# Kernel optimization log

Measured on AMD Instinct MI355X. Metric: run time of the kernel, lower is better.

## Reference

```python
import jax, jax.numpy as jnp
import numpy as np

B, T, D = 32, 4096, 256
P, K, L = 2, 17, 3
NH, HD, FF, HID = 8, 32, 2048, 128


def _ln(x, w, b):
    m = x.mean(-1, keepdims=True)
    v = ((x - m) ** 2).mean(-1, keepdims=True)
    return (x - m) * jax.lax.rsqrt(v + 1e-5) * w + b


def _refine(x, w1, b1, w2, b2):
    # x: (B,P,K,D). Vectorized all-pairs: pair[b,p,i,j] = concat(x_i, x_j); MLP; mean over j; residual.
    xi = jnp.broadcast_to(x[:, :, :, None, :], (B, P, K, K, D))
    xj = jnp.broadcast_to(x[:, :, None, :, :], (B, P, K, K, D))
    pair = jnp.concatenate([xi, xj], axis=-1)  # (B,P,K,K,2D)
    h = jax.nn.relu(pair @ w1.T + b1)
    y = (h @ w2.T + b2).mean(axis=3)  # (B,P,K,D)
    return y + x


def _forward(memory, person_q, key_q, sa_in_w, sa_in_b, sa_out_w, sa_out_b,
             ca_in_w, ca_in_b, ca_out_w, ca_out_b, ff1_w, ff1_b, ff2_w, ff2_b,
             ln1_w, ln1_b, ln2_w, ln2_b, ln3_w, ln3_b,
             r1_w1, r1_b1, r1_w2, r1_b2, r2_w1, r2_b1, r2_w2, r2_b2, fc_w, fc_b):
    scale = 1.0 / np.sqrt(HD).astype(np.float32)
    # tgt for person p = person_q[p] + key_q, all persons vectorized into axis P
    x = jnp.broadcast_to(person_q[None, :, None, :] + key_q[None, None, :, :], (B, P, K, D))
    for l in range(L):
        # --- self-attention over K keypoint queries (post-norm TransformerDecoderLayer) ---
        qkv = x @ sa_in_w[l].T + sa_in_b[l]
        q, k, v = jnp.split(qkv, 3, axis=-1)
        qh = q.reshape(B, P, K, NH, HD)
        kh = k.reshape(B, P, K, NH, HD)
        vh = v.reshape(B, P, K, NH, HD)
        a = jax.nn.softmax(jnp.einsum('bpqhd,bpkhd->bphqk', qh, kh) * scale, axis=-1)
        o = jnp.einsum('bphqk,bpkhd->bpqhd', a, vh).reshape(B, P, K, D)
        x = _ln(x + o @ sa_out_w[l].T + sa_out_b[l], ln1_w[l], ln1_b[l])
        # --- cross-attention to memory; memory K/V computed once, shared across persons ---
        q = x @ ca_in_w[l][:D].T + ca_in_b[l][:D]
        mk = memory @ ca_in_w[l][D:2 * D].T + ca_in_b[l][D:2 * D]
        mv = memory @ ca_in_w[l][2 * D:].T + ca_in_b[l][2 * D:]
        qh = q.reshape(B, P, K, NH, HD)
        kh = mk.reshape(B, T, NH, HD)
        vh = mv.reshape(B, T, NH, HD)
        a = jax.nn.softmax(jnp.einsum('bpqhd,bthd->bphqt', qh, kh) * scale, axis=-1)
        o = jnp.einsum('bphqt,bthd->bpqhd', a, vh).reshape(B, P, K, D)
        x = _ln(x + o @ ca_out_w[l].T + ca_out_b[l], ln2_w[l], ln2_b[l])
        # --- feed-forward (ReLU, dim_feedforward=2048 default) ---
        h = jax.nn.relu(x @ ff1_w[l].T + ff1_b[l])
        x = _ln(x + h @ ff2_w[l].T + ff2_b[l], ln3_w[l], ln3_b[l])
    x = _refine(x, r1_w1, r1_b1, r1_w2, r1_b2)
    x = _refine(x, r2_w1, r2_b1, r2_w2, r2_b2)
    return x @ fc_w.T + fc_b  # (B, P, K, 3)


def setup_inputs() -> dict:
    key = jax.random.key(0)
    ks = iter(jax.random.split(key, 48))

    def w(shape, s=0.02):
        return jax.random.normal(next(ks), shape, dtype=jnp.float32) * s

    inp = {
        'memory': jax.random.normal(next(ks), (B, T, D), dtype=jnp.float32),
        'person_q': jax.random.normal(next(ks), (P, D), dtype=jnp.float32),
        'key_q': jax.random.normal(next(ks), (K, D), dtype=jnp.float32),
        'sa_in_w': w((L, 3 * D, D)), 'sa_in_b': jnp.zeros((L, 3 * D)),
        'sa_out_w': w((L, D, D)), 'sa_out_b': jnp.zeros((L, D)),
        'ca_in_w': w((L, 3 * D, D)), 'ca_in_b': jnp.zeros((L, 3 * D)),
        'ca_out_w': w((L, D, D)), 'ca_out_b': jnp.zeros((L, D)),
        'ff1_w': w((L, FF, D)), 'ff1_b': jnp.zeros((L, FF)),
        'ff2_w': w((L, D, FF)), 'ff2_b': jnp.zeros((L, D)),
        'ln1_w': jnp.ones((L, D)), 'ln1_b': jnp.zeros((L, D)),
        'ln2_w': jnp.ones((L, D)), 'ln2_b': jnp.zeros((L, D)),
        'ln3_w': jnp.ones((L, D)), 'ln3_b': jnp.zeros((L, D)),
        'r1_w1': w((HID, 2 * D)), 'r1_b1': jnp.zeros((HID,)),
        'r1_w2': w((D, HID)), 'r1_b2': jnp.zeros((D,)),
        'r2_w1': w((HID, 2 * D)), 'r2_b1': jnp.zeros((HID,)),
        'r2_w2': w((D, HID)), 'r2_b2': jnp.zeros((D,)),
        'fc_w': w((3, D)), 'fc_b': jnp.zeros((3,)),
    }
    return inp


def reference(memory, person_q, key_q, sa_in_w, sa_in_b, sa_out_w, sa_out_b,
              ca_in_w, ca_in_b, ca_out_w, ca_out_b, ff1_w, ff1_b, ff2_w, ff2_b,
              ln1_w, ln1_b, ln2_w, ln2_b, ln3_w, ln3_b,
              r1_w1, r1_b1, r1_w2, r1_b2, r2_w1, r2_b1, r2_w2, r2_b2, fc_w, fc_b):
    return _forward(memory, person_q, key_q, sa_in_w, sa_in_b, sa_out_w, sa_out_b,
                    ca_in_w, ca_in_b, ca_out_w, ca_out_b, ff1_w, ff1_b, ff2_w, ff2_b,
                    ln1_w, ln1_b, ln2_w, ln2_b, ln3_w, ln3_b,
                    r1_w1, r1_b1, r1_w2, r1_b2, r2_w1, r2_b1, r2_w2, r2_b2, fc_w, fc_b)
```

## Files before the change

kernel.cpp:

```cpp
#include <hip/hip_runtime.h>
#include <stdint.h>

#define NB   32
#define TSEQ 4096
#define DD   256
#define PP   2
#define KK   17
#define LL   3
#define NHH  8
#define HDD  32
#define FFD  2048
#define HIDD 128
#define ROWS 1088
#define SCALE 0.17677669529663689f

typedef __attribute__((ext_vector_type(4))) float f32x4;
typedef __attribute__((ext_vector_type(8))) short bf16x8;

static __device__ __forceinline__ unsigned cvtpk(float lo, float hi) {
  unsigned r;
  asm volatile("v_cvt_pk_bf16_f32 %0, %1, %2" : "=v"(r) : "v"(lo), "v"(hi));
  return r;
}
static __device__ __forceinline__ unsigned short f2bf(float f) {
  unsigned int x = __float_as_uint(f);
  return (unsigned short)((x + 0x7fffu + ((x >> 16) & 1u)) >> 16);
}
static __device__ __forceinline__ void gload_lds16(const void* g, void* l) {
  __builtin_amdgcn_global_load_lds(
      (const __attribute__((address_space(1))) unsigned int*)g,
      (__attribute__((address_space(3))) unsigned int*)l, 16, 0, 0);
}

struct CvtJob { const float* src; unsigned short* dst; int n; };
struct CvtJobs8 { CvtJob j[8]; };
__global__ __launch_bounds__(256) void cvt_multi_kernel(CvtJobs8 jobs) {
#pragma unroll
  for (int jj = 0; jj < 8; ++jj) {
    const float* src = jobs.j[jj].src;
    unsigned short* dst = jobs.j[jj].dst;
    const int n8 = jobs.j[jj].n >> 3;
    for (int i = blockIdx.x * 256 + threadIdx.x; i < n8; i += gridDim.x * 256) {
      const float4 f0 = *reinterpret_cast<const float4*>(src + i * 8);
      const float4 f1 = *reinterpret_cast<const float4*>(src + i * 8 + 4);
      uint4 st;
      st.x = cvtpk(f0.x, f0.y); st.y = cvtpk(f0.z, f0.w);
      st.z = cvtpk(f1.x, f1.y); st.w = cvtpk(f1.z, f1.w);
      *reinterpret_cast<uint4*>(dst + i * 8) = st;
    }
  }
}

__global__ __launch_bounds__(256) void prep_small_kernel(
    const float* __restrict__ person_q, const float* __restrict__ key_q,
    const float* __restrict__ ca_in_w, const float* __restrict__ ca_in_b,
    const float* __restrict__ ca_out_w, const float* __restrict__ ca_out_b,
    float* __restrict__ x, unsigned short* __restrict__ x_bf,
    float* __restrict__ bqk, float* __restrict__ bvo) {
  const int bx = blockIdx.x, tid = threadIdx.x;
  if (bx < ROWS) {
    const int p = (bx / KK) & 1, k = bx % KK;
    const float v = person_q[p * DD + tid] + key_q[k * DD + tid];
    x[(size_t)bx * DD + tid] = v;
    x_bf[(size_t)bx * DD + tid] = f2bf(v);
  } else if (bx < ROWS + 24) {
    const int b2 = bx - ROWS;
    const int l = b2 >> 3, h = b2 & 7;
    const float* Wk = ca_in_w + (size_t)l * 196608 + (size_t)(256 + h * 32) * 256;
    const float* bq = ca_in_b + l * 768 + h * 32;
    float acc = 0.f;
#pragma unroll
    for (int j = 0; j < 32; ++j) acc += bq[j] * Wk[(size_t)j * 256 + tid];
    bqk[(size_t)l * 2048 + h * 256 + tid] = acc * SCALE;
  } else {
    const int l = bx - ROWS - 24;
    float acc = ca_out_b[l * 256 + tid];
    for (int j = 0; j < 256; ++j)
      acc += ca_out_w[(size_t)l * 65536 + (size_t)tid * 256 + j] * ca_in_b[l * 768 + 512 + j];
    bvo[l * 256 + tid] = acc;
  }
}

__global__ __launch_bounds__(256) void gemm_bf16_kernel(
    const unsigned short* __restrict__ Xbf, const unsigned short* __restrict__ Wbf,
    const float* __restrict__ bias, const float* __restrict__ R,
    float* __restrict__ Yf, unsigned short* __restrict__ Ybf,
    int M, int N, int K, int wstride, int relu) {
  __shared__ unsigned short Xs[64 * 64];
  __shared__ unsigned short Ws[64 * 64];
  const int tid = threadIdx.x, lane = tid & 63, w = tid >> 6;
  const int g = lane >> 4, q16 = lane & 15;
  const int m0 = blockIdx.y * 64, n0 = blockIdx.x * 64;
  f32x4 acc[4];
#pragma unroll
  for (int nt = 0; nt < 4; ++nt) acc[nt] = (f32x4){0.f, 0.f, 0.f, 0.f};

  for (int k0 = 0; k0 < K; k0 += 64) {
    __syncthreads();
#pragma unroll
    for (int j = 0; j < 2; ++j) {
      const int cc = w * 2 + j;
      const int row = cc * 8 + (lane >> 3);
      const int sc = (lane & 7) ^ (row & 7);
      gload_lds16(Xbf + (size_t)(m0 + row) * K + k0 + sc * 8, &Xs[cc * 512]);
      gload_lds16(Wbf + (size_t)(n0 + row) * wstride + k0 + sc * 8, &Ws[cc * 512]);
    }
    asm volatile("s_waitcnt vmcnt(0)" ::: "memory");
    __syncthreads();
    const int arow = w * 16 + q16;
#pragma unroll
    for (int ks = 0; ks < 2; ++ks) {
      const bf16x8 a = *reinterpret_cast<const bf16x8*>(
          &Xs[arow * 64 + ((((ks << 2) + g) ^ (arow & 7)) << 3)]);
#pragma unroll
      for (int nt = 0; nt < 4; ++nt) {
        const int brow = nt * 16 + q16;
        const bf16x8 bfr = *reinterpret_cast<const bf16x8*>(
            &Ws[brow * 64 + ((((ks << 2) + g) ^ (brow & 7)) << 3)]);
        acc[nt] = __builtin_amdgcn_mfma_f32_16x16x32_bf16(a, bfr, acc[nt], 0, 0, 0);
      }
    }
  }
#pragma unroll
  for (int nt = 0; nt < 4; ++nt) {
    const int n = n0 + nt * 16 + q16;
    const float bv = bias ? bias[n] : 0.f;
#pragma unroll
    for (int r = 0; r < 4; ++r) {
      const int m = m0 + w * 16 + g * 4 + r;
      float o = acc[nt][r] + bv;
      if (relu) o = fmaxf(o, 0.f);
      if (R) o += R[(size_t)m * N + n];
      if (Yf) Yf[(size_t)m * N + n] = o;
      if (Ybf) Ybf[(size_t)m * N + n] = f2bf(o);
    }
  }
}

__global__ __launch_bounds__(256) void gemm_bf16_sk_kernel(
    const unsigned short* __restrict__ Xbf, const unsigned short* __restrict__ Wbf,
    float* __restrict__ part, int M, int N, int K, int wstride, int kslice) {
  __shared__ unsigned short Xs[64 * 64];
  __shared__ unsigned short Ws[64 * 64];
  const int tid = threadIdx.x, lane = tid & 63, w = tid >> 6;
  const int g = lane >> 4, q16 = lane & 15;
  const int m0 = blockIdx.y * 64, n0 = blockIdx.x * 64;
  const int kz = blockIdx.z;
  const int kbeg = kz * kslice, kend = kbeg + kslice;
  f32x4 acc[4];
#pragma unroll
  for (int nt = 0; nt < 4; ++nt) acc[nt] = (f32x4){0.f, 0.f, 0.f, 0.f};

  for (int k0 = kbeg; k0 < kend; k0 += 64) {
    __syncthreads();
#pragma unroll
    for (int j = 0; j < 2; ++j) {
      const int cc = w * 2 + j;
      const int row = cc * 8 + (lane >> 3);
      const int sc = (lane & 7) ^ (row & 7);
      gload_lds16(Xbf + (size_t)(m0 + row) * K + k0 + sc * 8, &Xs[cc * 512]);
      gload_lds16(Wbf + (size_t)(n0 + row) * wstride + k0 + sc * 8, &Ws[cc * 512]);
    }
    asm volatile("s_waitcnt vmcnt(0)" ::: "memory");
    __syncthreads();
    const int arow = w * 16 + q16;
#pragma unroll
    for (int ks = 0; ks < 2; ++ks) {
      const bf16x8 a = *reinterpret_cast<const bf16x8*>(
          &Xs[arow * 64 + ((((ks << 2) + g) ^ (arow & 7)) << 3)]);
#pragma unroll
      for (int nt = 0; nt < 4; ++nt) {
        const int brow = nt * 16 + q16;
        const bf16x8 bfr = *reinterpret_cast<const bf16x8*>(
            &Ws[brow * 64 + ((((ks << 2) + g) ^ (brow & 7)) << 3)]);
        acc[nt] = __builtin_amdgcn_mfma_f32_16x16x32_bf16(a, bfr, acc[nt], 0, 0, 0);
      }
    }
  }
  float* pout = part + (size_t)kz * M * N;
#pragma unroll
  for (int nt = 0; nt < 4; ++nt) {
    const int n = n0 + nt * 16 + q16;
#pragma unroll
    for (int r = 0; r < 4; ++r) {
      const int m = m0 + w * 16 + g * 4 + r;
      pout[(size_t)m * N + n] = acc[nt][r];
    }
  }
}

__global__ __launch_bounds__(256) void ln_red_kernel(
    const float* __restrict__ xin, const float* __restrict__ parts, int np,
    const float* __restrict__ bias, const float* __restrict__ w,
    const float* __restrict__ b, float* __restrict__ xout,
    unsigned short* __restrict__ xout_bf) {
  const int row = blockIdx.x, tid = threadIdx.x;
  const size_t base = (size_t)row * DD + tid;
  float v = xin[base] + bias[tid];
  for (int p = 0; p < np; ++p) v += parts[(size_t)p * ROWS * DD + base];
  float s = v, s2 = v * v;
#pragma unroll
  for (int off = 32; off > 0; off >>= 1) {
    s += __shfl_down(s, off);
    s2 += __shfl_down(s2, off);
  }
  __shared__ float ps[4], ps2[4];
  if ((tid & 63) == 0) { ps[tid >> 6] = s; ps2[tid >> 6] = s2; }
  __syncthreads();
  const float st = ps[0] + ps[1] + ps[2] + ps[3];
  const float st2 = ps2[0] + ps2[1] + ps2[2] + ps2[3];
  const float mean = st * (1.f / 256.f);
  const float var = st2 * (1.f / 256.f) - mean * mean;
  const float inv = rsqrtf(var + 1e-5f);
  const float o = (v - mean) * inv * w[tid] + b[tid];
  xout[base] = o;
  xout_bf[base] = f2bf(o);
}

__global__ __launch_bounds__(256) void fc_kernel(
    const float* __restrict__ x, const float* __restrict__ fc_w,
    const float* __restrict__ fc_b, float* __restrict__ out) {
  const int row = blockIdx.x * 4 + (threadIdx.x >> 6);
  const int lane = threadIdx.x & 63;
  float xr[4];
#pragma unroll
  for (int j = 0; j < 4; ++j) xr[j] = x[(size_t)row * DD + lane + 64 * j];
#pragma unroll
  for (int o = 0; o < 3; ++o) {
    float s = 0.f;
#pragma unroll
    for (int j = 0; j < 4; ++j) s += xr[j] * fc_w[o * DD + lane + 64 * j];
#pragma unroll
    for (int off = 32; off > 0; off >>= 1) s += __shfl_down(s, off);
    if (lane == 0) out[(size_t)row * 3 + o] = s + fc_b[o];
  }
}

__global__ __launch_bounds__(64) void sa_attn_kernel(
    const float* __restrict__ qkv, unsigned short* __restrict__ attn_bf) {
  const int blk = blockIdx.x;
  const int h = blk & 7, bp = blk >> 3;
  const int rowbase = bp * KK;
  const int tid = threadIdx.x;
  __shared__ float qs[KK][36], ks[KK][36], vs[KK][36];
  __shared__ float ss[KK][20];
  __shared__ float lsum[KK];
  for (int i = tid; i < KK * HDD; i += 64) {
    const int r = i >> 5, d = i & 31;
    const size_t base = (size_t)(rowbase + r) * 768 + h * 32 + d;
    qs[r][d] = qkv[base];
    ks[r][d] = qkv[base + 256];
    vs[r][d] = qkv[base + 512];
  }
  __syncthreads();
  for (int i = tid; i < KK * KK; i += 64) {
    const int q = i / KK, k = i % KK;
    float s = 0.f;
#pragma unroll
    for (int d = 0; d < HDD; ++d) s += qs[q][d] * ks[k][d];
    ss[q][k] = s * SCALE;
  }
  __syncthreads();
  if (tid < KK) {
    float m = -1e30f;
    for (int k = 0; k < KK; ++k) m = fmaxf(m, ss[tid][k]);
    float l = 0.f;
    for (int k = 0; k < KK; ++k) { const float e = __expf(ss[tid][k] - m); ss[tid][k] = e; l += e; }
    lsum[tid] = l;
  }
  __syncthreads();
  for (int i = tid; i < KK * HDD; i += 64) {
    const int q = i >> 5, d = i & 31;
    float o = 0.f;
#pragma unroll
    for (int k = 0; k < KK; ++k) o += ss[q][k] * vs[k][d];
    attn_bf[(size_t)(rowbase + q) * DD + h * 32 + d] = f2bf(o / lsum[q]);
  }
}

__global__ __launch_bounds__(256) void wqkvo_kernel(
    const float* __restrict__ ca_in_w, const float* __restrict__ ca_out_w,
    unsigned short* __restrict__ Wqk_bf, unsigned short* __restrict__ Wvo_bf) {
  const int bx0 = blockIdx.x;
  if (bx0 < 6144) {
    const int l = bx0 >> 11, hc = bx0 & 2047;
    const int h = hc >> 8, c = hc & 255;
    const int d = threadIdx.x;
    const float* Wq = ca_in_w + (size_t)l * 196608 + (size_t)(h * 32) * 256;
    const float* Wk = ca_in_w + (size_t)l * 196608 + (size_t)(256 + h * 32) * 256;
    float acc = 0.f;
#pragma unroll
    for (int j = 0; j < 32; ++j) acc += Wk[(size_t)j * 256 + c] * Wq[(size_t)j * 256 + d];
    Wqk_bf[((size_t)l * 2048 + hc) * 256 + d] = f2bf(acc * SCALE);
  } else {
    const int bx = bx0 - 6144;
    const int h = bx & 7, dp = (bx >> 3) & 255, l = bx >> 11;
    const int c = threadIdx.x;
    const float* wout = ca_out_w + (size_t)l * 65536 + (size_t)dp * 256 + h * 32;
    const float* wv = ca_in_w + (size_t)l * 196608 + (size_t)(512 + h * 32) * 256 + c;
    float acc = 0.f;
#pragma unroll
    for (int j = 0; j < 32; ++j) acc += wout[j] * wv[(size_t)j * 256];
    Wvo_bf[((size_t)l * 256 + dp) * 2048 + h * 256 + c] = f2bf(acc);
  }
}

__global__ __launch_bounds__(256) void prep_mem_kernel(
    const float* __restrict__ memory, unsigned short* __restrict__ mem_bf,
    unsigned short* __restrict__ memT) {
  const int b = blockIdx.x >> 6, tc = blockIdx.x & 63;
  const int tid = threadIdx.x;
  __shared__ unsigned short tile[64][264];
  for (int it = 0; it < 8; ++it) {
    const int idx = it * 256 + tid;
    const int t = idx >> 5, c8 = (idx & 31) << 3;
    const size_t goff = ((size_t)b * TSEQ + tc * 64 + t) * DD + c8;
    const float4 f0 = *reinterpret_cast<const float4*>(memory + goff);
    const float4 f1 = *reinterpret_cast<const float4*>(memory + goff + 4);
    uint4 st;
    st.x = cvtpk(f0.x, f0.y); st.y = cvtpk(f0.z, f0.w);
    st.z = cvtpk(f1.x, f1.y); st.w = cvtpk(f1.z, f1.w);
    *reinterpret_cast<uint4*>(&tile[t][c8]) = st;
    *reinterpret_cast<uint4*>(mem_bf + goff) = st;
  }
  __syncthreads();
  for (int it = 0; it < 8; ++it) {
    const int idx = it * 256 + tid;
    const int c = idx >> 3, t8 = (idx & 7) << 3;
    union { unsigned short v[8]; uint4 u; } pk;
#pragma unroll
    for (int j = 0; j < 8; ++j) pk.v[j] = tile[t8 + j][c];
    *reinterpret_cast<uint4*>(&memT[((size_t)b * DD + c) * TSEQ + tc * 64 + t8]) = pk.u;
  }
}

#define PS3 72
__global__ __launch_bounds__(256, 2) void ca_fused_kernel(
    const unsigned short* __restrict__ qkeff_bf, const unsigned short* __restrict__ mem_bf,
    const unsigned short* __restrict__ memT,
    float* __restrict__ o_part, float* __restrict__ m_part, float* __restrict__ l_part) {
  const int h = blockIdx.x >> 6;
  const int b = (blockIdx.x >> 1) & 31;
  const int half = blockIdx.x & 1;
  const int tid = threadIdx.x;
  const int lane = tid & 63, w = tid >> 6;
  const int g = lane >> 4, q16 = lane & 15;

  __shared__ unsigned short mem_lds[64 * 256];
  __shared__ unsigned short memT_lds[256 * 64];
  __shared__ unsigned short p_lds[48 * PS3];
  __shared__ float red_m[4 * 48];
  __shared__ float red_l[4 * 48];
  __shared__ float r_lds[48];

  bf16x8 bq[3][8];
#pragma unroll
  for (int qt = 0; qt < 3; ++qt) {
    const int ql = qt * 16 + q16;
    if (ql < 34) {
      const unsigned short* qbase = qkeff_bf + (size_t)(b * 34 + ql) * 2048 + h * 256;
#pragma unroll
      for (int ks = 0; ks < 8; ++ks)
        bq[qt][ks] = *reinterpret_cast<const bf16x8*>(qbase + ks * 32 + g * 8);
    } else {
#pragma unroll
      for (int ks = 0; ks < 8; ++ks) bq[qt][ks] = (bf16x8){0, 0, 0, 0, 0, 0, 0, 0};
    }
  }

  f32x4 ctx[3][4];
#pragma unroll
  for (int mt = 0; mt < 3; ++mt)
#pragma unroll
    for (int nt = 0; nt < 4; ++nt) ctx[mt][nt] = (f32x4){0.f, 0.f, 0.f, 0.f};
  float m_run[3] = {-1e30f, -1e30f, -1e30f};
  float l_run[3] = {0.f, 0.f, 0.f};

  const unsigned short* membb = mem_bf + (size_t)b * TSEQ * DD;
  const unsigned short* memTb = memT + (size_t)b * DD * TSEQ;

  for (int tile = 0; tile < 32; ++tile) {
    const int tbase = half * 2048 + tile * 64;
    __syncthreads();

#pragma unroll
    for (int j = 0; j < 8; ++j) {
      const int cc = w * 8 + j;
      const int trow = cc * 2 + (lane >> 5);
      const int sc = (lane & 31) ^ (trow & 7);
      gload_lds16(membb + (size_t)(tbase + trow) * DD + sc * 8, &mem_lds[cc * 512]);
    }
#pragma unroll
    for (int j = 0; j < 8; ++j) {
      const int cc = w * 8 + j;
      const int crow = cc * 8 + (lane >> 3);
      const int sc = (lane & 7) ^ (crow & 7);
      gload_lds16(memTb + (size_t)crow * TSEQ + tbase + sc * 8, &memT_lds[cc * 512]);
    }
    asm volatile("s_waitcnt vmcnt(0)" ::: "memory");
    __syncthreads();

    f32x4 sacc[3];
#pragma unroll
    for (int qt = 0; qt < 3; ++qt) sacc[qt] = (f32x4){0.f, 0.f, 0.f, 0.f};
    {
      const int arow = w * 16 + q16;
      __builtin_amdgcn_s_setprio(1);
#pragma unroll
      for (int ks = 0; ks < 8; ++ks) {
        const bf16x8 af = *reinterpret_cast<const bf16x8*>(
            &mem_lds[arow * 256 + ((((ks << 2) + g) ^ (arow & 7)) << 3)]);
#pragma unroll
        for (int qt = 0; qt < 3; ++qt)
          sacc[qt] = __builtin_amdgcn_mfma_f32_16x16x32_bf16(af, bq[qt][ks], sacc[qt], 0, 0, 0);
      }
      __builtin_amdgcn_s_setprio(0);
    }

#pragma unroll
    for (int qt = 0; qt < 3; ++qt) {
      float v = fmaxf(fmaxf(sacc[qt][0], sacc[qt][1]), fmaxf(sacc[qt][2], sacc[qt][3]));
      v = fmaxf(v, __shfl_xor(v, 16));
      v = fmaxf(v, __shfl_xor(v, 32));
      if (lane < 16) red_m[w * 48 + qt * 16 + lane] = v;
    }
    __syncthreads();

    float rfac[3], mnew[3];
#pragma unroll
    for (int qt = 0; qt < 3; ++qt) {
      const int q = qt * 16 + q16;
      const float tmax = fmaxf(fmaxf(red_m[q], red_m[48 + q]),
                               fmaxf(red_m[96 + q], red_m[144 + q]));
      mnew[qt] = fmaxf(m_run[qt], tmax);
      rfac[qt] = __expf(m_run[qt] - mnew[qt]);
      m_run[qt] = mnew[qt];
    }
    if (w == 0 && lane < 16) {
#pragma unroll
      for (int qt = 0; qt < 3; ++qt) r_lds[qt * 16 + lane] = rfac[qt];
    }

#pragma unroll
    for (int qt = 0; qt < 3; ++qt) {
      const float p0 = __expf(sacc[qt][0] - mnew[qt]);
      const float p1 = __expf(sacc[qt][1] - mnew[qt]);
      const float p2 = __expf(sacc[qt][2] - mnew[qt]);
      const float p3 = __expf(sacc[qt][3] - mnew[qt]);
      const int prow = (qt * 16 + q16) * PS3 + w * 16 + g * 4;
      *reinterpret_cast<unsigned*>(&p_lds[prow]) = cvtpk(p0, p1);
      *reinterpret_cast<unsigned*>(&p_lds[prow + 2]) = cvtpk(p2, p3);
      float ps = (p0 + p1) + (p2 + p3);
      ps += __shfl_xor(ps, 16);
      ps += __shfl_xor(ps, 32);
      if (lane < 16) red_l[w * 48 + qt * 16 + lane] = ps;
    }
    __syncthreads();

#pragma unroll
    for (int qt = 0; qt < 3; ++qt) {
      const int q = qt * 16 + q16;
      l_run[qt] = l_run[qt] * rfac[qt] +
                  ((red_l[q] + red_l[48 + q]) + (red_l[96 + q] + red_l[144 + q]));
    }
#pragma unroll
    for (int mt = 0; mt < 3; ++mt)
#pragma unroll
      for (int r = 0; r < 4; ++r) {
        const float rr = r_lds[mt * 16 + g * 4 + r];
#pragma unroll
        for (int nt = 0; nt < 4; ++nt) ctx[mt][nt][r] *= rr;
      }

    bf16x8 pf[3][2];
#pragma unroll
    for (int mt = 0; mt < 3; ++mt)
#pragma unroll
      for (int ks2 = 0; ks2 < 2; ++ks2)
        pf[mt][ks2] = *reinterpret_cast<const bf16x8*>(
            &p_lds[(mt * 16 + q16) * PS3 + ks2 * 32 + g * 8]);
    __builtin_amdgcn_s_setprio(1);
#pragma unroll
    for (int nt = 0; nt < 4; ++nt) {
      const int c = w * 64 + nt * 16 + q16;
#pragma unroll
      for (int ks2 = 0; ks2 < 2; ++ks2) {
        const bf16x8 bT = *reinterpret_cast<const bf16x8*>(
            &memT_lds[c * 64 + ((((ks2 << 2) + g) ^ (c & 7)) << 3)]);
#pragma unroll
        for (int mt = 0; mt < 3; ++mt)
          ctx[mt][nt] = __builtin_amdgcn_mfma_f32_16x16x32_bf16(pf[mt][ks2], bT,
                                                                ctx[mt][nt], 0, 0, 0);
      }
    }
    __builtin_amdgcn_s_setprio(0);
  }

#pragma unroll
  for (int mt = 0; mt < 3; ++mt)
#pragma unroll
    for (int r = 0; r < 4; ++r) {
      const int q = mt * 16 + g * 4 + r;
      if (q < 34) {
        const size_t orow = (size_t)(half * ROWS + b * 34 + q) * 2048;
#pragma unroll
        for (int nt = 0; nt < 4; ++nt)
          o_part[orow + h * 256 + w * 64 + nt * 16 + q16] = ctx[mt][nt][r];
      }
    }
  if (w == 0 && lane < 16) {
#pragma unroll
    for (int qt = 0; qt < 3; ++qt) {
      const int q = qt * 16 + lane;
      if (q < 34) {
        const size_t idx = (size_t)(half * ROWS + b * 34 + q) * 8 + h;
        m_part[idx] = m_run[qt];
        l_part[idx] = l_run[qt];
      }
    }
  }
}

__global__ __launch_bounds__(256) void ca_combine_kernel(
    const float* __restrict__ o_part, const float* __restrict__ m_part,
    const float* __restrict__ l_part, unsigned short* __restrict__ ctx_bf) {
  const int row = blockIdx.x, c = threadIdx.x;
#pragma unroll
  for (int h = 0; h < NHH; ++h) {
    const float m0 = m_part[(size_t)row * 8 + h];
    const float m1 = m_part[(size_t)(ROWS + row) * 8 + h];
    const float l0 = l_part[(size_t)row * 8 + h];
    const float l1 = l_part[(size_t)(ROWS + row) * 8 + h];
    const float M = fmaxf(m0, m1);
    const float w0 = __expf(m0 - M), w1 = __expf(m1 - M);
    const float denom = l0 * w0 + l1 * w1;
    const float o0 = o_part[(size_t)row * 2048 + h * 256 + c];
    const float o1 = o_part[(size_t)(ROWS + row) * 2048 + h * 256 + c];
    ctx_bf[(size_t)row * 2048 + h * 256 + c] = f2bf((o0 * w0 + o1 * w1) / denom);
  }
}

__global__ __launch_bounds__(256) void pairmean_kernel(
    const float* __restrict__ u, const float* __restrict__ v,
    unsigned short* __restrict__ hbar_bf) {
  const int bp = blockIdx.x, tid = threadIdx.x;
  const int r0 = bp * KK;
  __shared__ float us[KK][132], vs[KK][132];
  for (int i = tid; i < KK * HIDD; i += 256) {
    const int r = i >> 7, f = i & 127;
    us[r][f] = u[(size_t)(r0 + r) * HIDD + f];
    vs[r][f] = v[(size_t)(r0 + r) * HIDD + f];
  }
  __syncthreads();
  for (int i = tid; i < KK * HIDD; i += 256) {
    const int r = i >> 7, f = i & 127;
    float s = 0.f;
#pragma unroll
    for (int j = 0; j < KK; ++j) s += fmaxf(us[r][f] + vs[j][f], 0.f);
    hbar_bf[(size_t)(r0 + r) * HIDD + f] = f2bf(s * (1.0f / 17.0f));
  }
}

static void gemm_bf(const unsigned short* X, const unsigned short* W, const float* bias,
                    const float* R, float* Yf, unsigned short* Ybf, int M, int N, int K,
                    int wstride, int relu, hipStream_t s) {
  dim3 g(N / 64, M / 64);
  gemm_bf16_kernel<<<g, 256, 0, s>>>(X, W, bias, R, Yf, Ybf, M, N, K, wstride, relu);
}
static void gemm_sk(const unsigned short* X, const unsigned short* W, float* part,
                    int M, int N, int K, int wstride, int ksplit, hipStream_t s) {
  dim3 g(N / 64, M / 64, ksplit);
  gemm_bf16_sk_kernel<<<g, 256, 0, s>>>(X, W, part, M, N, K, wstride, K / ksplit);
}

extern "C" void kernel_launch(void* const* d_in, const int* in_sizes, int n_in,
                              void* d_out, int out_size, void* d_ws, size_t ws_size,
                              hipStream_t stream) {
  const float* memory   = (const float*)d_in[0];
  const float* person_q = (const float*)d_in[1];
  const float* key_q    = (const float*)d_in[2];
  const float* sa_in_w  = (const float*)d_in[3];
  const float* sa_in_b  = (const float*)d_in[4];
  const float* sa_out_w = (const float*)d_in[5];
  const float* sa_out_b = (const float*)d_in[6];
  const float* ca_in_w  = (const float*)d_in[7];
  const float* ca_in_b  = (const float*)d_in[8];
  const float* ca_out_w = (const float*)d_in[9];
  const float* ca_out_b = (const float*)d_in[10];
  const float* ff1_w = (const float*)d_in[11];
  const float* ff1_b = (const float*)d_in[12];
  const float* ff2_w = (const float*)d_in[13];
  const float* ff2_b = (const float*)d_in[14];
  const float* ln1_w = (const float*)d_in[15];
  const float* ln1_b = (const float*)d_in[16];
  const float* ln2_w = (const float*)d_in[17];
  const float* ln2_b = (const float*)d_in[18];
  const float* ln3_w = (const float*)d_in[19];
  const float* ln3_b = (const float*)d_in[20];
  const float* r1_w1 = (const float*)d_in[21];
  const float* r1_b1 = (const float*)d_in[22];
  const float* r1_w2 = (const float*)d_in[23];
  const float* r1_b2 = (const float*)d_in[24];
  const float* r2_w1 = (const float*)d_in[25];
  const float* r2_b1 = (const float*)d_in[26];
  const float* r2_w2 = (const float*)d_in[27];
  const float* r2_b2 = (const float*)d_in[28];
  const float* fc_w  = (const float*)d_in[29];
  const float* fc_b  = (const float*)d_in[30];
  float* out = (float*)d_out;

  char* wsb = (char*)d_ws;
  size_t off = 0;
  auto alloc = [&](size_t bytes) -> char* {
    char* p = wsb + off;
    off += (bytes + 255) & ~(size_t)255;
    return p;
  };
  float* x      = (float*)alloc((size_t)ROWS * DD * 4);
  float* qkv    = (float*)alloc((size_t)ROWS * 768 * 4);
  float* parts  = (float*)alloc((size_t)4 * ROWS * DD * 4);
  float* bvo    = (float*)alloc(3 * 256 * 4);
  float* bqk    = (float*)alloc((size_t)3 * 2048 * 4);
  float* ubuf   = (float*)alloc((size_t)ROWS * HIDD * 4);
  float* vbuf   = (float*)alloc((size_t)ROWS * HIDD * 4);
  float* o_part = (float*)alloc((size_t)2 * ROWS * 2048 * 4);
  float* m_part = (float*)alloc((size_t)2 * ROWS * 8 * 4);
  float* l_part = (float*)alloc((size_t)2 * ROWS * 8 * 4);
  unsigned short* x_bf     = (unsigned short*)alloc((size_t)ROWS * DD * 2);
  unsigned short* attn_bf  = (unsigned short*)alloc((size_t)ROWS * DD * 2);
  unsigned short* hff_bf   = (unsigned short*)alloc((size_t)ROWS * 2048 * 2);
  unsigned short* ctx_bf   = (unsigned short*)alloc((size_t)ROWS * 2048 * 2);
  unsigned short* qkeff_bf = (unsigned short*)alloc((size_t)ROWS * 2048 * 2);
  unsigned short* hbar_bf  = (unsigned short*)alloc((size_t)ROWS * HIDD * 2);
  unsigned short* mem_bf   = (unsigned short*)alloc((size_t)NB * TSEQ * DD * 2);
  unsigned short* memT     = (unsigned short*)alloc((size_t)NB * TSEQ * DD * 2);
  unsigned short* sa_in_bf  = (unsigned short*)alloc((size_t)3 * 768 * 256 * 2);
  unsigned short* sa_out_bf = (unsigned short*)alloc((size_t)3 * 256 * 256 * 2);
  unsigned short* Wqk_bf   = (unsigned short*)alloc((size_t)3 * 2048 * 256 * 2);
  unsigned short* ff1_bf   = (unsigned short*)alloc((size_t)3 * 2048 * 256 * 2);
  unsigned short* ff2_bf   = (unsigned short*)alloc((size_t)3 * 256 * 2048 * 2);
  unsigned short* Wvo_bf   = (unsigned short*)alloc((size_t)3 * 256 * 2048 * 2);
  unsigned short* r1w1_bf  = (unsigned short*)alloc((size_t)HIDD * 512 * 2);
  unsigned short* r1w2_bf  = (unsigned short*)alloc((size_t)DD * HIDD * 2);
  unsigned short* r2w1_bf  = (unsigned short*)alloc((size_t)HIDD * 512 * 2);
  unsigned short* r2w2_bf  = (unsigned short*)alloc((size_t)DD * HIDD * 2);

  prep_mem_kernel<<<NB * 64, 256, 0, stream>>>(memory, mem_bf, memT);
  CvtJobs8 jobs;
  jobs.j[0] = {sa_in_w,  sa_in_bf,  3 * 768 * 256};
  jobs.j[1] = {sa_out_w, sa_out_bf, 3 * 256 * 256};
  jobs.j[2] = {ff1_w,    ff1_bf,    3 * 2048 * 256};
  jobs.j[3] = {ff2_w,    ff2_bf,    3 * 256 * 2048};
  jobs.j[4] = {r1_w1,    r1w1_bf,   HIDD * 512};
  jobs.j[5] = {r1_w2,    r1w2_bf,   DD * HIDD};
  jobs.j[6] = {r2_w1,    r2w1_bf,   HIDD * 512};
  jobs.j[7] = {r2_w2,    r2w2_bf,   DD * HIDD};
  cvt_multi_kernel<<<1024, 256, 0, stream>>>(jobs);
  wqkvo_kernel<<<12288, 256, 0, stream>>>(ca_in_w, ca_out_w, Wqk_bf, Wvo_bf);
  prep_small_kernel<<<ROWS + 24 + 3, 256, 0, stream>>>(
      person_q, key_q, ca_in_w, ca_in_b, ca_out_w, ca_out_b, x, x_bf, bqk, bvo);

  for (int l = 0; l < LL; ++l) {
    gemm_bf(x_bf, sa_in_bf + (size_t)l * 768 * 256, sa_in_b + l * 768, nullptr,
            qkv, nullptr, ROWS, 768, 256, 256, 0, stream);
    sa_attn_kernel<<<512, 64, 0, stream>>>(qkv, attn_bf);
    gemm_sk(attn_bf, sa_out_bf + (size_t)l * 256 * 256, parts,
            ROWS, 256, 256, 256, 2, stream);
    ln_red_kernel<<<ROWS, 256, 0, stream>>>(x, parts, 2, sa_out_b + l * 256,
                                            ln1_w + l * 256, ln1_b + l * 256, x, x_bf);
    gemm_bf(x_bf, Wqk_bf + (size_t)l * 2048 * 256, bqk + l * 2048, nullptr,
            nullptr, qkeff_bf, ROWS, 2048, 256, 256, 0, stream);
    ca_fused_kernel<<<512, 256, 0, stream>>>(qkeff_bf, mem_bf, memT, o_part, m_part, l_part);
    ca_combine_kernel<<<ROWS, 256, 0, stream>>>(o_part, m_part, l_part, ctx_bf);
    gemm_sk(ctx_bf, Wvo_bf + (size_t)l * 256 * 2048, parts,
            ROWS, 256, 2048, 2048, 4, stream);
    ln_red_kernel<<<ROWS, 256, 0, stream>>>(x, parts, 4, bvo + l * 256,
                                            ln2_w + l * 256, ln2_b + l * 256, x, x_bf);
    gemm_bf(x_bf, ff1_bf + (size_t)l * 2048 * 256, ff1_b + l * 2048, nullptr,
            nullptr, hff_bf, ROWS, 2048, 256, 256, 1, stream);
    gemm_sk(hff_bf, ff2_bf + (size_t)l * 256 * 2048, parts,
            ROWS, 256, 2048, 2048, 4, stream);
    ln_red_kernel<<<ROWS, 256, 0, stream>>>(x, parts, 4, ff2_b + l * 256,
                                            ln3_w + l * 256, ln3_b + l * 256, x, x_bf);
  }

  const unsigned short* rw1_bf[2] = {r1w1_bf, r2w1_bf};
  const unsigned short* rw2_bf[2] = {r1w2_bf, r2w2_bf};
  const float* rb1[2] = {r1_b1, r2_b1};
  const float* rb2[2] = {r1_b2, r2_b2};
  for (int r = 0; r < 2; ++r) {
    gemm_bf(x_bf, rw1_bf[r], rb1[r], nullptr, ubuf, nullptr,
            ROWS, 128, 256, 512, 0, stream);
    gemm_bf(x_bf, rw1_bf[r] + 256, nullptr, nullptr, vbuf, nullptr,
            ROWS, 128, 256, 512, 0, stream);
    pairmean_kernel<<<64, 256, 0, stream>>>(ubuf, vbuf, hbar_bf);
    gemm_bf(hbar_bf, rw2_bf[r], rb2[r], x, x, x_bf,
            ROWS, 256, 128, 128, 0, stream);
  }

  fc_kernel<<<ROWS / 4, 256, 0, stream>>>(x, fc_w, fc_b, out);
}
```

Baseline: 662.8 us.

## Defer online-softmax rescaling in cross-attention and merge refine U/V GEMMs

In the fused cross-attention kernel, the running max is now kept unchanged whenever every lane's new tile max exceeds it by at most 8. In that case the exp rescale of the context accumulators and the running sum is skipped, saving exps, LDS traffic and multiplies in the inner loop. Separately, the two refine-MLP first-layer GEMMs (the u and v halves) are packed into one N=256 weight and run as a single GEMM, with the bias moved into the pairmean kernel. This removes one launch per refine stage. The cost is a slightly larger bf16 range for the unnormalized probabilities (up to e^8) and an extra packing step in the weight-prep kernel.

After: 640.1 us (median of 2 runs). 1.04x faster.

```diff
diff --git a/kernel.cpp b/kernel.cpp
--- a/kernel.cpp
+++ b/kernel.cpp
@@ -280,7 +280,9 @@
 
 __global__ __launch_bounds__(256) void wqkvo_kernel(
     const float* __restrict__ ca_in_w, const float* __restrict__ ca_out_w,
-    unsigned short* __restrict__ Wqk_bf, unsigned short* __restrict__ Wvo_bf) {
+    const float* __restrict__ r1_w1, const float* __restrict__ r2_w1,
+    unsigned short* __restrict__ Wqk_bf, unsigned short* __restrict__ Wvo_bf,
+    unsigned short* __restrict__ rpack_bf) {
   const int bx0 = blockIdx.x;
   if (bx0 < 6144) {
     const int l = bx0 >> 11, hc = bx0 & 2047;
@@ -292,7 +294,7 @@
 #pragma unroll
     for (int j = 0; j < 32; ++j) acc += Wk[(size_t)j * 256 + c] * Wq[(size_t)j * 256 + d];
     Wqk_bf[((size_t)l * 2048 + hc) * 256 + d] = f2bf(acc * SCALE);
-  } else {
+  } else if (bx0 < 12288) {
     const int bx = bx0 - 6144;
     const int h = bx & 7, dp = (bx >> 3) & 255, l = bx >> 11;
     const int c = threadIdx.x;
@@ -302,6 +304,13 @@
 #pragma unroll
     for (int j = 0; j < 32; ++j) acc += wout[j] * wv[(size_t)j * 256];
     Wvo_bf[((size_t)l * 256 + dp) * 2048 + h * 256 + c] = f2bf(acc);
+  } else {
+    const int bx2 = bx0 - 12288;
+    const int rr = bx2 >> 8, n = bx2 & 255;
+    const float* w1 = rr ? r2_w1 : r1_w1;
+    const float v = (n < 128) ? w1[(size_t)n * 512 + threadIdx.x]
+                              : w1[(size_t)(n - 128) * 512 + 256 + threadIdx.x];
+    rpack_bf[(size_t)rr * 65536 + (size_t)n * 256 + threadIdx.x] = f2bf(v);
   }
 }
 
@@ -426,27 +435,36 @@
     }
     __syncthreads();
 
-    float rfac[3], mnew[3];
+    float tmax[3];
 #pragma unroll
     for (int qt = 0; qt < 3; ++qt) {
       const int q = qt * 16 + q16;
-      const float tmax = fmaxf(fmaxf(red_m[q], red_m[48 + q]),
-                               fmaxf(red_m[96 + q], red_m[144 + q]));
-      mnew[qt] = fmaxf(m_run[qt], tmax);
-      rfac[qt] = __expf(m_run[qt] - mnew[qt]);
-      m_run[qt] = mnew[qt];
-    }
-    if (w == 0 && lane < 16) {
-#pragma unroll
-      for (int qt = 0; qt < 3; ++qt) r_lds[qt * 16 + lane] = rfac[qt];
+      tmax[qt] = fmaxf(fmaxf(red_m[q], red_m[48 + q]),
+                       fmaxf(red_m[96 + q], red_m[144 + q]));
+    }
+    const float dmax = fmaxf(fmaxf(tmax[0] - m_run[0], tmax[1] - m_run[1]),
+                             tmax[2] - m_run[2]);
+    const bool defer = __all(dmax <= 8.0f);
+    float rfac[3] = {1.f, 1.f, 1.f};
+    if (!defer) {
+#pragma unroll
+      for (int qt = 0; qt < 3; ++qt) {
+        const float mnew = fmaxf(m_run[qt], tmax[qt]);
+        rfac[qt] = __expf(m_run[qt] - mnew);
+        m_run[qt] = mnew;
+      }
+      if (w == 0 && lane < 16) {
+#pragma unroll
+        for (int qt = 0; qt < 3; ++qt) r_lds[qt * 16 + lane] = rfac[qt];
+      }
     }
 
 #pragma unroll
     for (int qt = 0; qt < 3; ++qt) {
-      const float p0 = __expf(sacc[qt][0] - mnew[qt]);
-      const float p1 = __expf(sacc[qt][1] - mnew[qt]);
-      const float p2 = __expf(sacc[qt][2] - mnew[qt]);
-      const float p3 = __expf(sacc[qt][3] - mnew[qt]);
+      const float p0 = __expf(sacc[qt][0] - m_run[qt]);
+      const float p1 = __expf(sacc[qt][1] - m_run[qt]);
+      const float p2 = __expf(sacc[qt][2] - m_run[qt]);
+      const float p3 = __expf(sacc[qt][3] - m_run[qt]);
       const int prow = (qt * 16 + q16) * PS3 + w * 16 + g * 4;
       *reinterpret_cast<unsigned*>(&p_lds[prow]) = cvtpk(p0, p1);
       *reinterpret_cast<unsigned*>(&p_lds[prow + 2]) = cvtpk(p2, p3);
@@ -460,17 +478,19 @@
 #pragma unroll
     for (int qt = 0; qt < 3; ++qt) {
       const int q = qt * 16 + q16;
-      l_run[qt] = l_run[qt] * rfac[qt] +
-                  ((red_l[q] + red_l[48 + q]) + (red_l[96 + q] + red_l[144 + q]));
-    }
-#pragma unroll
-    for (int mt = 0; mt < 3; ++mt)
-#pragma unroll
-      for (int r = 0; r < 4; ++r) {
-        const float rr = r_lds[mt * 16 + g * 4 + r];
-#pragma unroll
-        for (int nt = 0; nt < 4; ++nt) ctx[mt][nt][r] *= rr;
-      }
+      const float ssum = (red_l[q] + red_l[48 + q]) + (red_l[96 + q] + red_l[144 + q]);
+      l_run[qt] = defer ? (l_run[qt] + ssum) : (l_run[qt] * rfac[qt] + ssum);
+    }
+    if (!defer) {
+#pragma unroll
+      for (int mt = 0; mt < 3; ++mt)
+#pragma unroll
+        for (int r = 0; r < 4; ++r) {
+          const float rr = r_lds[mt * 16 + g * 4 + r];
+#pragma unroll
+          for (int nt = 0; nt < 4; ++nt) ctx[mt][nt][r] *= rr;
+        }
+    }
 
     bf16x8 pf[3][2];
 #pragma unroll
@@ -541,22 +561,25 @@
 }
 
 __global__ __launch_bounds__(256) void pairmean_kernel(
-    const float* __restrict__ u, const float* __restrict__ v,
+    const float* __restrict__ uv, const float* __restrict__ b1,
     unsigned short* __restrict__ hbar_bf) {
   const int bp = blockIdx.x, tid = threadIdx.x;
   const int r0 = bp * KK;
   __shared__ float us[KK][132], vs[KK][132];
+  __shared__ float b1s[128];
+  if (tid < 128) b1s[tid] = b1[tid];
   for (int i = tid; i < KK * HIDD; i += 256) {
     const int r = i >> 7, f = i & 127;
-    us[r][f] = u[(size_t)(r0 + r) * HIDD + f];
-    vs[r][f] = v[(size_t)(r0 + r) * HIDD + f];
+    us[r][f] = uv[(size_t)(r0 + r) * 256 + f];
+    vs[r][f] = uv[(size_t)(r0 + r) * 256 + 128 + f];
   }
   __syncthreads();
   for (int i = tid; i < KK * HIDD; i += 256) {
     const int r = i >> 7, f = i & 127;
+    const float ub = us[r][f] + b1s[f];
     float s = 0.f;
 #pragma unroll
-    for (int j = 0; j < KK; ++j) s += fmaxf(us[r][f] + vs[j][f], 0.f);
+    for (int j = 0; j < KK; ++j) s += fmaxf(ub + vs[j][f], 0.f);
     hbar_bf[(size_t)(r0 + r) * HIDD + f] = f2bf(s * (1.0f / 17.0f));
   }
 }
@@ -621,8 +644,7 @@
   float* parts  = (float*)alloc((size_t)4 * ROWS * DD * 4);
   float* bvo    = (float*)alloc(3 * 256 * 4);
   float* bqk    = (float*)alloc((size_t)3 * 2048 * 4);
-  float* ubuf   = (float*)alloc((size_t)ROWS * HIDD * 4);
-  float* vbuf   = (float*)alloc((size_t)ROWS * HIDD * 4);
+  float* uvbuf  = (float*)alloc((size_t)ROWS * 256 * 4);
   float* o_part = (float*)alloc((size_t)2 * ROWS * 2048 * 4);
   float* m_part = (float*)alloc((size_t)2 * ROWS * 8 * 4);
   float* l_part = (float*)alloc((size_t)2 * ROWS * 8 * 4);
@@ -640,9 +662,8 @@
   unsigned short* ff1_bf   = (unsigned short*)alloc((size_t)3 * 2048 * 256 * 2);
   unsigned short* ff2_bf   = (unsigned short*)alloc((size_t)3 * 256 * 2048 * 2);
   unsigned short* Wvo_bf   = (unsigned short*)alloc((size_t)3 * 256 * 2048 * 2);
-  unsigned short* r1w1_bf  = (unsigned short*)alloc((size_t)HIDD * 512 * 2);
+  unsigned short* rpack_bf = (unsigned short*)alloc((size_t)2 * 256 * 256 * 2);
   unsigned short* r1w2_bf  = (unsigned short*)alloc((size_t)DD * HIDD * 2);
-  unsigned short* r2w1_bf  = (unsigned short*)alloc((size_t)HIDD * 512 * 2);
   unsigned short* r2w2_bf  = (unsigned short*)alloc((size_t)DD * HIDD * 2);
 
   prep_mem_kernel<<<NB * 64, 256, 0, stream>>>(memory, mem_bf, memT);
@@ -651,12 +672,13 @@
   jobs.j[1] = {sa_out_w, sa_out_bf, 3 * 256 * 256};
   jobs.j[2] = {ff1_w,    ff1_bf,    3 * 2048 * 256};
   jobs.j[3] = {ff2_w,    ff2_bf,    3 * 256 * 2048};
-  jobs.j[4] = {r1_w1,    r1w1_bf,   HIDD * 512};
-  jobs.j[5] = {r1_w2,    r1w2_bf,   DD * HIDD};
-  jobs.j[6] = {r2_w1,    r2w1_bf,   HIDD * 512};
-  jobs.j[7] = {r2_w2,    r2w2_bf,   DD * HIDD};
+  jobs.j[4] = {r1_w2,    r1w2_bf,   DD * HIDD};
+  jobs.j[5] = {r2_w2,    r2w2_bf,   DD * HIDD};
+  jobs.j[6] = {r1_w2,    r1w2_bf,   0};
+  jobs.j[7] = {r2_w2,    r2w2_bf,   0};
   cvt_multi_kernel<<<1024, 256, 0, stream>>>(jobs);
-  wqkvo_kernel<<<12288, 256, 0, stream>>>(ca_in_w, ca_out_w, Wqk_bf, Wvo_bf);
+  wqkvo_kernel<<<12800, 256, 0, stream>>>(ca_in_w, ca_out_w, r1_w1, r2_w1,
+                                          Wqk_bf, Wvo_bf, rpack_bf);
   prep_small_kernel<<<ROWS + 24 + 3, 256, 0, stream>>>(
       person_q, key_q, ca_in_w, ca_in_b, ca_out_w, ca_out_b, x, x_bf, bqk, bvo);
 
@@ -684,16 +706,13 @@
                                             ln3_w + l * 256, ln3_b + l * 256, x, x_bf);
   }
 
-  const unsigned short* rw1_bf[2] = {r1w1_bf, r2w1_bf};
   const unsigned short* rw2_bf[2] = {r1w2_bf, r2w2_bf};
   const float* rb1[2] = {r1_b1, r2_b1};
   const float* rb2[2] = {r1_b2, r2_b2};
   for (int r = 0; r < 2; ++r) {
-    gemm_bf(x_bf, rw1_bf[r], rb1[r], nullptr, ubuf, nullptr,
-            ROWS, 128, 256, 512, 0, stream);
-    gemm_bf(x_bf, rw1_bf[r] + 256, nullptr, nullptr, vbuf, nullptr,
-            ROWS, 128, 256, 512, 0, stream);
-    pairmean_kernel<<<64, 256, 0, stream>>>(ubuf, vbuf, hbar_bf);
+    gemm_bf(x_bf, rpack_bf + (size_t)r * 65536, nullptr, nullptr, uvbuf, nullptr,
+            ROWS, 256, 256, 256, 0, stream);
+    pairmean_kernel<<<64, 256, 0, stream>>>(uvbuf, rb1[r], hbar_bf);
     gemm_bf(hbar_bf, rw2_bf[r], rb2[r], x, x, x_bf,
             ROWS, 256, 128, 128, 0, stream);
   }
```
